# Kernel tuning notes

Measured on AMD Instinct MI355X. Metric: run time of the kernel, lower is better.

Reference implementation:

```python
import jax, jax.numpy as jnp
import numpy as np

N = 5000       # num_vertices
E = 160000     # num edges (avg degree 32)
F = 256        # per-node feature width
T = 8          # T_train iterative steps
LR_X = 0.1
N_INTERNAL = 2500


def setup_inputs() -> dict:
    key = jax.random.key(0)
    k1, k2, k3 = jax.random.split(key, 3)
    values = jax.random.normal(k1, (N, F), dtype=jnp.float32)
    w = jax.random.normal(k2, (N, N), dtype=jnp.float32) * 0.05  # nn.init.normal_(std=0.05)
    edge_index = jax.random.randint(k3, (2, E), 0, N, dtype=jnp.int64)
    internal_indices = jnp.arange(N_INTERNAL, dtype=jnp.int64)
    return {"values": values, "w": w, "edge_index": edge_index,
            "internal_indices": internal_indices}


def reference(values, w, edge_index, internal_indices):
    # PyG source_to_target flow: x_j = x[edge_index[0]], aggregate at edge_index[1]
    src, dst = edge_index[0], edge_index[1]
    w_e = w[src, dst][:, None]            # [E,1] gathered edge weights
    lr = jnp.float32(LR_X)

    def step(vals, _):
        # prediction_mp: scatter_add of w * tanh(x_j) into dst
        pred = jax.ops.segment_sum(w_e * jnp.tanh(vals[src]), dst, num_segments=N)
        err = vals - pred                 # errors[:] = values - prediction
        # gradx_mp: scatter_add of w * dfdx(err_j); dfdx(tanh) = 1 - tanh^2
        t = jnp.tanh(err[src])
        gradx = err - jax.ops.segment_sum(w_e * (1.0 - t * t), dst, num_segments=N)
        # values[internal] -= lr_x * dEdx[internal]  (train=True mask)
        vals = vals.at[internal_indices].add(-lr * gradx[internal_indices])
        return vals, None

    vals, _ = jax.lax.scan(step, values, None, length=T)
    return vals
```

## Files before the change

### kernel.cpp

```cpp
#include <hip/hip_runtime.h>
#include <hip/hip_bf16.h>

#define FDIM 256
#define CHUNK 64
#define T_STEPS 8
#define LR_X 0.1f
#define EXT_BIT (1 << 24)

__device__ __forceinline__ float ftanh(float x) {
    float ax = fabsf(x);
    float z  = __expf(-2.f * ax);
    float t  = (1.f - z) * __builtin_amdgcn_rcpf(1.f + z);
    return copysignf(t, x);
}


__global__ void k_count(const int* __restrict__ dst, int* __restrict__ cnt, int E) {
    int e = blockIdx.x * blockDim.x + threadIdx.x;
    if (e < E) atomicAdd(&cnt[dst[e]], 1);
}

__global__ __launch_bounds__(1024) void k_scan(int* cntcur, int* start, int n) {
    __shared__ int sdata[1024];
    int running = 0;
    for (int base = 0; base < n + 1; base += 1024) {
        int i = base + (int)threadIdx.x;
        int v = (i < n) ? cntcur[i] : 0;
        sdata[threadIdx.x] = v;
        __syncthreads();
        for (int off = 1; off < 1024; off <<= 1) {
            int t = ((int)threadIdx.x >= off) ? sdata[threadIdx.x - off] : 0;
            __syncthreads();
            sdata[threadIdx.x] += t;
            __syncthreads();
        }
        int incl = sdata[threadIdx.x];
        int total = sdata[1023];
        if (i <= n) {
            int excl = running + incl - v;
            start[i] = excl;
            if (i < n) cntcur[i] = excl;
        }
        running += total;
        __syncthreads();
    }
}

__global__ void k_fill_slots(const int* __restrict__ dst, int* __restrict__ cursor,
                             int* __restrict__ eidT, int E) {
    int e = blockIdx.x * blockDim.x + threadIdx.x;
    if (e >= E) return;
    int p = atomicAdd(&cursor[dst[e]], 1);
    eidT[p] = e;
}

__global__ void k_key(const int* __restrict__ eidT, const int* __restrict__ src,
                      int* __restrict__ keyT, int* __restrict__ colS, int E, int NI) {
    int p = blockIdx.x * blockDim.x + threadIdx.x;
    if (p >= E) return;
    int e  = eidT[p];
    int sc = src[e];
    keyT[p] = ((sc >= NI) ? EXT_BIT : 0) | e;
    colS[p] = sc;
}

__global__ __launch_bounds__(256) void k_rank_scatter(
    const int* __restrict__ keyT, const int* __restrict__ colS,
    const int* __restrict__ start, const float* __restrict__ w,
    int* __restrict__ col, float* __restrict__ wv, int* __restrict__ mid,
    int nRows, int N) {
    const int wid  = (int)((blockIdx.x * blockDim.x + threadIdx.x) >> 6);
    const int lane = (int)(threadIdx.x & 63);
    if (wid >= nRows) return;
    const int s = start[wid], e = start[wid + 1];
    int nInt = 0;
    for (int i = s + lane; i < e; i += 64) {
        const int myk = keyT[i];
        int rank = 0;
        for (int j = s; j < e; ++j)
            rank += (keyT[j] < myk) ? 1 : 0;
        const int pos = s + rank;
        const int sc  = colS[i];
        col[pos] = sc * FDIM;
        wv[pos]  = w[(size_t)sc * N + wid];
        nInt += (myk < EXT_BIT) ? 1 : 0;
    }
    for (int off = 1; off < 64; off <<= 1)
        nInt += __shfl_xor(nInt, off);
    if (lane == 0) mid[wid] = s + nInt;
}

__global__ void k_init(const float* __restrict__ vin, float* __restrict__ vals,
                       __hip_bfloat16* __restrict__ th, int n) {
    int i = blockIdx.x * blockDim.x + threadIdx.x;
    if (i < n) {
        float v = vin[i];
        vals[i] = v;
        th[i] = __float2bfloat16(ftanh(v));
    }
}

__global__ __launch_bounds__(FDIM) void k_predc(
    const int* __restrict__ mid, const int* __restrict__ start,
    const int* __restrict__ col, const float* __restrict__ wv,
    const __hip_bfloat16* __restrict__ th, float* __restrict__ predc) {
    const int d = blockIdx.x;
    const int f = (int)threadIdx.x;
    const int m = mid[d], e = start[d + 1];
    __shared__ int   s_col[CHUNK];
    __shared__ float s_w[CHUNK];
    float acc = 0.f;
    for (int base = m; base < e; base += CHUNK) {
        const int cnt = min(CHUNK, e - base);
        __syncthreads();
        if (f < cnt) { s_col[f] = col[base + f]; s_w[f] = wv[base + f]; }
        __syncthreads();
        for (int j = 0; j < cnt; ++j)
            acc = fmaf(s_w[j], __bfloat162float(th[s_col[j] + f]), acc);
    }
    predc[d * FDIM + f] = acc;
}


__global__ __launch_bounds__(FDIM) void k_pred(
    const int* __restrict__ start, const int* __restrict__ mid,
    const int* __restrict__ col, const float* __restrict__ wv,
    const float* __restrict__ vals, const float* __restrict__ predc,
    const __hip_bfloat16* __restrict__ th, float* __restrict__ err,
    __hip_bfloat16* __restrict__ dd, int NI) {
    const int d = blockIdx.x;
    const int f = (int)threadIdx.x;
    const int s = start[d], m = mid[d];
    __shared__ int   s_col[CHUNK];
    __shared__ float s_w[CHUNK];
    float acc = 0.f;
    for (int base = s; base < m; base += CHUNK) {
        const int cnt = min(CHUNK, m - base);
        __syncthreads();
        if (f < cnt) { s_col[f] = col[base + f]; s_w[f] = wv[base + f]; }
        __syncthreads();
        for (int j = 0; j < cnt; ++j)
            acc = fmaf(s_w[j], __bfloat162float(th[s_col[j] + f]), acc);
    }
    const int idx = d * FDIM + f;
    const float er = vals[idx] - (predc[idx] + acc);
    if (d < NI) err[idx] = er;
    const float u = ftanh(er);
    dd[idx] = __float2bfloat16(1.f - u * u);
}

__global__ __launch_bounds__(FDIM) void k_grad(
    const int* __restrict__ start, const int* __restrict__ col,
    const float* __restrict__ wv, const float* __restrict__ err,
    const __hip_bfloat16* __restrict__ dd, float* __restrict__ vals,
    __hip_bfloat16* __restrict__ th) {
    const int d = blockIdx.x;
    const int f = (int)threadIdx.x;
    const int s = start[d], e = start[d + 1];
    __shared__ int   s_col[CHUNK];
    __shared__ float s_w[CHUNK];
    float g = 0.f;
    for (int base = s; base < e; base += CHUNK) {
        const int cnt = min(CHUNK, e - base);
        __syncthreads();
        if (f < cnt) { s_col[f] = col[base + f]; s_w[f] = wv[base + f]; }
        __syncthreads();
        for (int j = 0; j < cnt; ++j)
            g = fmaf(s_w[j], __bfloat162float(dd[s_col[j] + f]), g);
    }
    const int idx = d * FDIM + f;
    const float nv = vals[idx] - LR_X * (err[idx] - g);
    vals[idx] = nv;
    th[idx] = __float2bfloat16(ftanh(nv));
}


extern "C" void kernel_launch(void* const* d_in, const int* in_sizes, int n_in,
                              void* d_out, int out_size, void* d_ws, size_t ws_size,
                              hipStream_t stream) {
    const float* values = (const float*)d_in[0];
    const float* w      = (const float*)d_in[1];
    const int*   edge   = (const int*)d_in[2];
    const int NF = in_sizes[0];
    const int N  = NF / FDIM;
    const int E  = in_sizes[2] / 2;
    const int NI = in_sizes[3];
    const int* srcp = edge;
    const int* dstp = edge + E;
    float* vals = (float*)d_out;

    char* ws = (char*)d_ws;
    size_t off = 0;
    auto alloc = [&](size_t bytes) {
        void* p = ws + off;
        off = (off + bytes + 255) & ~(size_t)255;
        return p;
    };
    int*   start = (int*)  alloc((size_t)(N + 1) * sizeof(int));
    int*   cur   = (int*)  alloc((size_t)N * sizeof(int));
    int*   mid   = (int*)  alloc((size_t)N * sizeof(int));
    int*   eidT  = (int*)  alloc((size_t)E * sizeof(int));
    int*   keyT  = (int*)  alloc((size_t)E * sizeof(int));
    int*   colS  = (int*)  alloc((size_t)E * sizeof(int));
    int*   col   = (int*)  alloc((size_t)E * sizeof(int));
    float* wv    = (float*)alloc((size_t)E * sizeof(float));
    __hip_bfloat16* th = (__hip_bfloat16*)alloc((size_t)NF * sizeof(__hip_bfloat16));
    __hip_bfloat16* dd = (__hip_bfloat16*)alloc((size_t)NF * sizeof(__hip_bfloat16));
    float* err   = (float*)alloc((size_t)NF * sizeof(float));
    float* predc = (float*)alloc((size_t)NF * sizeof(float));
    (void)ws_size; (void)n_in; (void)out_size;

    hipMemsetAsync(cur, 0, (size_t)N * sizeof(int), stream);
    const int gE = (E + 255) / 256;
    k_count<<<gE, 256, 0, stream>>>(dstp, cur, E);
    k_scan<<<1, 1024, 0, stream>>>(cur, start, N);
    k_fill_slots<<<gE, 256, 0, stream>>>(dstp, cur, eidT, E);
    k_key<<<gE, 256, 0, stream>>>(eidT, srcp, keyT, colS, E, NI);
    k_rank_scatter<<<(N + 3) / 4, 256, 0, stream>>>(keyT, colS, start, w, col, wv, mid, N, N);
    k_init<<<(NF + 255) / 256, 256, 0, stream>>>(values, vals, th, NF);
    k_predc<<<N, FDIM, 0, stream>>>(mid, start, col, wv, th, predc);

    for (int t = 0; t < T_STEPS; ++t) {
        k_pred<<<N, FDIM, 0, stream>>>(start, mid, col, wv, vals, predc, th, err, dd, NI);
        k_grad<<<NI, FDIM, 0, stream>>>(start, col, wv, err, dd, vals, th);
    }
}
```

Measured before the change: 242.4 us.

## Vectorize gathers to bf16x2, use wave shuffles, fuse setup and first pred kernels

Each thread now handles two features as bf16x2/float2, halving block size to 128, and edge indices and weights are broadcast with wave shuffles instead of shared memory with block barriers. Two accumulator pairs break the FMA dependency chain. The setup kernels are fused: count with init, fill with key generation, and the external-neighbor precompute with the first prediction step. This aims to cut launch count, barrier overhead and the number of load instructions per gathered row, at the cost of fewer threads per block.

After: 241.3 us. No clear change (-0.5%).

```diff
diff --git a/kernel.cpp b/kernel.cpp
--- a/kernel.cpp
+++ b/kernel.cpp
@@ -2,10 +2,12 @@
 #include <hip/hip_bf16.h>
 
 #define FDIM 256
-#define CHUNK 64
+#define F2   128
 #define T_STEPS 8
 #define LR_X 0.1f
 #define EXT_BIT (1 << 24)
+
+typedef __hip_bfloat162 bf2;
 
 __device__ __forceinline__ float ftanh(float x) {
     float ax = fabsf(x);
@@ -13,11 +15,29 @@
     float t  = (1.f - z) * __builtin_amdgcn_rcpf(1.f + z);
     return copysignf(t, x);
 }
-
-
-__global__ void k_count(const int* __restrict__ dst, int* __restrict__ cnt, int E) {
-    int e = blockIdx.x * blockDim.x + threadIdx.x;
-    if (e < E) atomicAdd(&cnt[dst[e]], 1);
+__device__ __forceinline__ float2 bf22f(const bf2 v) {
+    return make_float2(__bfloat162float(v.x), __bfloat162float(v.y));
+}
+__device__ __forceinline__ bf2 f22bf(float x, float y) {
+    bf2 r; r.x = __float2bfloat16(x); r.y = __float2bfloat16(y); return r;
+}
+
+
+__global__ void k_count_init(const int* __restrict__ dst, int* __restrict__ cnt, int E,
+                             const float* __restrict__ vin, float* __restrict__ vals,
+                             bf2* __restrict__ th2, int NF2, int gE) {
+    const int b = (int)blockIdx.x;
+    if (b < gE) {
+        int e = b * 256 + (int)threadIdx.x;
+        if (e < E) atomicAdd(&cnt[dst[e]], 1);
+    } else {
+        int i = (b - gE) * 256 + (int)threadIdx.x;
+        if (i < NF2) {
+            float2 v = ((const float2*)vin)[i];
+            ((float2*)vals)[i] = v;
+            th2[i] = f22bf(ftanh(v.x), ftanh(v.y));
+        }
+    }
 }
 
 __global__ __launch_bounds__(1024) void k_scan(int* cntcur, int* start, int n) {
@@ -46,20 +66,13 @@
     }
 }
 
-__global__ void k_fill_slots(const int* __restrict__ dst, int* __restrict__ cursor,
-                             int* __restrict__ eidT, int E) {
+__global__ void k_fill(const int* __restrict__ src, const int* __restrict__ dst,
+                       int* __restrict__ cursor, int* __restrict__ keyT,
+                       int* __restrict__ colS, int E, int NI) {
     int e = blockIdx.x * blockDim.x + threadIdx.x;
     if (e >= E) return;
+    int sc = src[e];
     int p = atomicAdd(&cursor[dst[e]], 1);
-    eidT[p] = e;
-}
-
-__global__ void k_key(const int* __restrict__ eidT, const int* __restrict__ src,
-                      int* __restrict__ keyT, int* __restrict__ colS, int E, int NI) {
-    int p = blockIdx.x * blockDim.x + threadIdx.x;
-    if (p >= E) return;
-    int e  = eidT[p];
-    int sc = src[e];
     keyT[p] = ((sc >= NI) ? EXT_BIT : 0) | e;
     colS[p] = sc;
 }
@@ -81,7 +94,7 @@
             rank += (keyT[j] < myk) ? 1 : 0;
         const int pos = s + rank;
         const int sc  = colS[i];
-        col[pos] = sc * FDIM;
+        col[pos] = sc * F2;
         wv[pos]  = w[(size_t)sc * N + wid];
         nInt += (myk < EXT_BIT) ? 1 : 0;
     }
@@ -90,88 +103,97 @@
     if (lane == 0) mid[wid] = s + nInt;
 }
 
-__global__ void k_init(const float* __restrict__ vin, float* __restrict__ vals,
-                       __hip_bfloat16* __restrict__ th, int n) {
-    int i = blockIdx.x * blockDim.x + threadIdx.x;
-    if (i < n) {
-        float v = vin[i];
-        vals[i] = v;
-        th[i] = __float2bfloat16(ftanh(v));
-    }
-}
-
-__global__ __launch_bounds__(FDIM) void k_predc(
-    const int* __restrict__ mid, const int* __restrict__ start,
+
+__device__ __forceinline__ void gather_acc(
     const int* __restrict__ col, const float* __restrict__ wv,
-    const __hip_bfloat16* __restrict__ th, float* __restrict__ predc) {
-    const int d = blockIdx.x;
-    const int f = (int)threadIdx.x;
-    const int m = mid[d], e = start[d + 1];
-    __shared__ int   s_col[CHUNK];
-    __shared__ float s_w[CHUNK];
-    float acc = 0.f;
-    for (int base = m; base < e; base += CHUNK) {
-        const int cnt = min(CHUNK, e - base);
-        __syncthreads();
-        if (f < cnt) { s_col[f] = col[base + f]; s_w[f] = wv[base + f]; }
-        __syncthreads();
-        for (int j = 0; j < cnt; ++j)
-            acc = fmaf(s_w[j], __bfloat162float(th[s_col[j] + f]), acc);
-    }
-    predc[d * FDIM + f] = acc;
-}
-
-
-__global__ __launch_bounds__(FDIM) void k_pred(
+    const bf2* __restrict__ src2, int s, int e, int lane, int f,
+    float& ax, float& ay, float& bx, float& by) {
+    for (int base = s; base < e; base += 64) {
+        const int n = min(64, e - base);
+        int c = 0; float ww = 0.f;
+        if (lane < n) { c = col[base + lane]; ww = wv[base + lane]; }
+        int j = 0;
+        for (; j + 2 <= n; j += 2) {
+            const int   c0 = __shfl(c, j),  c1 = __shfl(c, j + 1);
+            const float w0 = __shfl(ww, j), w1 = __shfl(ww, j + 1);
+            const float2 t0 = bf22f(src2[c0 + f]);
+            const float2 t1 = bf22f(src2[c1 + f]);
+            ax = fmaf(w0, t0.x, ax); ay = fmaf(w0, t0.y, ay);
+            bx = fmaf(w1, t1.x, bx); by = fmaf(w1, t1.y, by);
+        }
+        for (; j < n; ++j) {
+            const int c0 = __shfl(c, j); const float w0 = __shfl(ww, j);
+            const float2 t0 = bf22f(src2[c0 + f]);
+            ax = fmaf(w0, t0.x, ax); ay = fmaf(w0, t0.y, ay);
+        }
+    }
+}
+
+__global__ __launch_bounds__(F2) void k_pred_first(
     const int* __restrict__ start, const int* __restrict__ mid,
     const int* __restrict__ col, const float* __restrict__ wv,
-    const float* __restrict__ vals, const float* __restrict__ predc,
-    const __hip_bfloat16* __restrict__ th, float* __restrict__ err,
-    __hip_bfloat16* __restrict__ dd, int NI) {
-    const int d = blockIdx.x;
+    const float2* __restrict__ vals2, float2* __restrict__ predc2,
+    const bf2* __restrict__ th2, float2* __restrict__ err2,
+    bf2* __restrict__ dd2, int NI) {
+    const int d = (int)blockIdx.x;
     const int f = (int)threadIdx.x;
+    const int lane = f & 63;
+    const int s = start[d], m = mid[d], e = start[d + 1];
+    float ix = 0.f, iy = 0.f, jx = 0.f, jy = 0.f;
+    float xx = 0.f, xy = 0.f, yx = 0.f, yy = 0.f;
+    gather_acc(col, wv, th2, s, m, lane, f, ix, iy, jx, jy);
+    gather_acc(col, wv, th2, m, e, lane, f, xx, xy, yx, yy);
+    const int idx = d * F2 + f;
+    const float pcx = xx + yx, pcy = xy + yy;
+    predc2[idx] = make_float2(pcx, pcy);
+    const float2 v = vals2[idx];
+    const float ex = v.x - (pcx + ix + jx);
+    const float ey = v.y - (pcy + iy + jy);
+    if (d < NI) err2[idx] = make_float2(ex, ey);
+    const float ux = ftanh(ex), uy = ftanh(ey);
+    dd2[idx] = f22bf(1.f - ux * ux, 1.f - uy * uy);
+}
+
+__global__ __launch_bounds__(F2) void k_pred(
+    const int* __restrict__ start, const int* __restrict__ mid,
+    const int* __restrict__ col, const float* __restrict__ wv,
+    const float2* __restrict__ vals2, const float2* __restrict__ predc2,
+    const bf2* __restrict__ th2, float2* __restrict__ err2,
+    bf2* __restrict__ dd2, int NI) {
+    const int d = (int)blockIdx.x;
+    const int f = (int)threadIdx.x;
+    const int lane = f & 63;
     const int s = start[d], m = mid[d];
-    __shared__ int   s_col[CHUNK];
-    __shared__ float s_w[CHUNK];
-    float acc = 0.f;
-    for (int base = s; base < m; base += CHUNK) {
-        const int cnt = min(CHUNK, m - base);
-        __syncthreads();
-        if (f < cnt) { s_col[f] = col[base + f]; s_w[f] = wv[base + f]; }
-        __syncthreads();
-        for (int j = 0; j < cnt; ++j)
-            acc = fmaf(s_w[j], __bfloat162float(th[s_col[j] + f]), acc);
-    }
-    const int idx = d * FDIM + f;
-    const float er = vals[idx] - (predc[idx] + acc);
-    if (d < NI) err[idx] = er;
-    const float u = ftanh(er);
-    dd[idx] = __float2bfloat16(1.f - u * u);
-}
-
-__global__ __launch_bounds__(FDIM) void k_grad(
+    float ax = 0.f, ay = 0.f, bx = 0.f, by = 0.f;
+    gather_acc(col, wv, th2, s, m, lane, f, ax, ay, bx, by);
+    const int idx = d * F2 + f;
+    const float2 pc = predc2[idx];
+    const float2 v  = vals2[idx];
+    const float ex = v.x - (pc.x + ax + bx);
+    const float ey = v.y - (pc.y + ay + by);
+    if (d < NI) err2[idx] = make_float2(ex, ey);
+    const float ux = ftanh(ex), uy = ftanh(ey);
+    dd2[idx] = f22bf(1.f - ux * ux, 1.f - uy * uy);
+}
+
+__global__ __launch_bounds__(F2) void k_grad(
     const int* __restrict__ start, const int* __restrict__ col,
-    const float* __restrict__ wv, const float* __restrict__ err,
-    const __hip_bfloat16* __restrict__ dd, float* __restrict__ vals,
-    __hip_bfloat16* __restrict__ th) {
-    const int d = blockIdx.x;
+    const float* __restrict__ wv, const float2* __restrict__ err2,
+    const bf2* __restrict__ dd2, float2* __restrict__ vals2,
+    bf2* __restrict__ th2) {
+    const int d = (int)blockIdx.x;
     const int f = (int)threadIdx.x;
+    const int lane = f & 63;
     const int s = start[d], e = start[d + 1];
-    __shared__ int   s_col[CHUNK];
-    __shared__ float s_w[CHUNK];
-    float g = 0.f;
-    for (int base = s; base < e; base += CHUNK) {
-        const int cnt = min(CHUNK, e - base);
-        __syncthreads();
-        if (f < cnt) { s_col[f] = col[base + f]; s_w[f] = wv[base + f]; }
-        __syncthreads();
-        for (int j = 0; j < cnt; ++j)
-            g = fmaf(s_w[j], __bfloat162float(dd[s_col[j] + f]), g);
-    }
-    const int idx = d * FDIM + f;
-    const float nv = vals[idx] - LR_X * (err[idx] - g);
-    vals[idx] = nv;
-    th[idx] = __float2bfloat16(ftanh(nv));
+    float ax = 0.f, ay = 0.f, bx = 0.f, by = 0.f;
+    gather_acc(col, wv, dd2, s, e, lane, f, ax, ay, bx, by);
+    const int idx = d * F2 + f;
+    const float2 er = err2[idx];
+    const float2 v  = vals2[idx];
+    const float nx = v.x - LR_X * (er.x - (ax + bx));
+    const float ny = v.y - LR_X * (er.y - (ay + by));
+    vals2[idx] = make_float2(nx, ny);
+    th2[idx] = f22bf(ftanh(nx), ftanh(ny));
 }
 
 
@@ -185,6 +207,7 @@
     const int N  = NF / FDIM;
     const int E  = in_sizes[2] / 2;
     const int NI = in_sizes[3];
+    const int NF2 = NF / 2;
     const int* srcp = edge;
     const int* dstp = edge + E;
     float* vals = (float*)d_out;
@@ -199,29 +222,33 @@
     int*   start = (int*)  alloc((size_t)(N + 1) * sizeof(int));
     int*   cur   = (int*)  alloc((size_t)N * sizeof(int));
     int*   mid   = (int*)  alloc((size_t)N * sizeof(int));
-    int*   eidT  = (int*)  alloc((size_t)E * sizeof(int));
     int*   keyT  = (int*)  alloc((size_t)E * sizeof(int));
     int*   colS  = (int*)  alloc((size_t)E * sizeof(int));
     int*   col   = (int*)  alloc((size_t)E * sizeof(int));
     float* wv    = (float*)alloc((size_t)E * sizeof(float));
-    __hip_bfloat16* th = (__hip_bfloat16*)alloc((size_t)NF * sizeof(__hip_bfloat16));
-    __hip_bfloat16* dd = (__hip_bfloat16*)alloc((size_t)NF * sizeof(__hip_bfloat16));
+    bf2*   th2   = (bf2*)  alloc((size_t)NF2 * sizeof(bf2));
+    bf2*   dd2   = (bf2*)  alloc((size_t)NF2 * sizeof(bf2));
     float* err   = (float*)alloc((size_t)NF * sizeof(float));
     float* predc = (float*)alloc((size_t)NF * sizeof(float));
     (void)ws_size; (void)n_in; (void)out_size;
 
+    float2* vals2  = (float2*)vals;
+    float2* err2   = (float2*)err;
+    float2* predc2 = (float2*)predc;
+
     hipMemsetAsync(cur, 0, (size_t)N * sizeof(int), stream);
-    const int gE = (E + 255) / 256;
-    k_count<<<gE, 256, 0, stream>>>(dstp, cur, E);
+    const int gE   = (E + 255) / 256;
+    const int gNF2 = (NF2 + 255) / 256;
+    k_count_init<<<gE + gNF2, 256, 0, stream>>>(dstp, cur, E, values, vals, th2, NF2, gE);
     k_scan<<<1, 1024, 0, stream>>>(cur, start, N);
-    k_fill_slots<<<gE, 256, 0, stream>>>(dstp, cur, eidT, E);
-    k_key<<<gE, 256, 0, stream>>>(eidT, srcp, keyT, colS, E, NI);
+    k_fill<<<gE, 256, 0, stream>>>(srcp, dstp, cur, keyT, colS, E, NI);
     k_rank_scatter<<<(N + 3) / 4, 256, 0, stream>>>(keyT, colS, start, w, col, wv, mid, N, N);
-    k_init<<<(NF + 255) / 256, 256, 0, stream>>>(values, vals, th, NF);
-    k_predc<<<N, FDIM, 0, stream>>>(mid, start, col, wv, th, predc);
 
     for (int t = 0; t < T_STEPS; ++t) {
-        k_pred<<<N, FDIM, 0, stream>>>(start, mid, col, wv, vals, predc, th, err, dd, NI);
-        k_grad<<<NI, FDIM, 0, stream>>>(start, col, wv, err, dd, vals, th);
-    }
-}
+        if (t == 0)
+            k_pred_first<<<N, F2, 0, stream>>>(start, mid, col, wv, vals2, predc2, th2, err2, dd2, NI);
+        else
+            k_pred<<<N, F2, 0, stream>>>(start, mid, col, wv, vals2, predc2, th2, err2, dd2, NI);
+        k_grad<<<NI, F2, 0, stream>>>(start, col, wv, err2, dd2, vals2, th2);
+    }
+}
```
